# Optimization experiments

Hardware: AMD Instinct MI355X
Metric: run time of the kernel (lower is better)

## Reference

```python
import jax, jax.numpy as jnp
import numpy as np

B, S, D, H, WS = 2, 4096, 768, 12, 256
HD = D // H
NW = S // WS
EPS = 1e-5


def layernorm(x, g, b):
    mu = jnp.mean(x, axis=-1, keepdims=True)
    var = jnp.mean(jnp.square(x - mu), axis=-1, keepdims=True)
    return (x - mu) * jax.lax.rsqrt(var + EPS) * g + b


def setup_inputs() -> dict:
    key = jax.random.key(0)
    ks = jax.random.split(key, 8)
    s = 0.02
    return {
        "x": jax.random.normal(ks[0], (B, S, D), dtype=jnp.float32),
        "Wq": jax.random.normal(ks[1], (D, D), dtype=jnp.float32) * s,
        "bq": jnp.zeros((D,), jnp.float32),
        "Wk": jax.random.normal(ks[2], (D, D), dtype=jnp.float32) * s,
        "bk": jnp.zeros((D,), jnp.float32),
        "Wv": jax.random.normal(ks[3], (D, D), dtype=jnp.float32) * s,
        "bv": jnp.zeros((D,), jnp.float32),
        "Wo": jax.random.normal(ks[4], (D, D), dtype=jnp.float32) * s,
        "bo": jnp.zeros((D,), jnp.float32),
        "ln1_g": jnp.ones((D,), jnp.float32),
        "ln1_b": jnp.zeros((D,), jnp.float32),
        "W1": jax.random.normal(ks[5], (D, 4 * D), dtype=jnp.float32) * s,
        "b1": jnp.zeros((4 * D,), jnp.float32),
        "W2": jax.random.normal(ks[6], (4 * D, D), dtype=jnp.float32) * s,
        "b2": jnp.zeros((D,), jnp.float32),
        "ln2_g": jnp.ones((D,), jnp.float32),
        "ln2_b": jnp.zeros((D,), jnp.float32),
    }


def _attn(h, Wq, bq, Wk, bk, Wv, bv, Wo, bo):
    q = (h @ Wq + bq).reshape(B, S, H, HD)
    k = (h @ Wk + bk).reshape(B, S, H, HD)
    v = (h @ Wv + bv).reshape(B, S, H, HD)
    # split into windows: [B, NW, WS, H, HD]
    kb = k.reshape(B, NW, WS, H, HD)
    vb = v.reshape(B, NW, WS, H, HD)
    qw = jnp.moveaxis(q.reshape(B, NW, WS, H, HD), 1, 0)  # [NW, B, WS, H, HD]
    inv = 1.0 / np.sqrt(HD).astype(np.float32)

    def step(carry, qi_i):
        qi, i = qi_i  # qi: [B, WS, H, HD]
        # per key-window scores: [B, H, NW, WSq, WSk]
        scores = jnp.einsum('bqhd,bjkhd->bhjqk', qi, kb) * inv
        attn = jax.nn.softmax(scores, axis=-1)  # per-block softmax (as in source)
        mask = (jnp.arange(NW) <= i).astype(attn.dtype)  # block-causal, include own window
        attn = attn * mask[None, None, :, None, None]
        ctx = jnp.einsum('bhjqk,bjkhd->bqhd', attn, vb)  # sum over key windows
        return carry, ctx

    _, ctxs = jax.lax.scan(step, None, (qw, jnp.arange(NW)))
    ctx = jnp.moveaxis(ctxs, 0, 1).reshape(B, S, D)
    return ctx @ Wo + bo


def reference(x, Wq, bq, Wk, bk, Wv, bv, Wo, bo, ln1_g, ln1_b, W1, b1, W2, b2, ln2_g, ln2_b):
    attn_out = _attn(layernorm(x, ln1_g, ln1_b), Wq, bq, Wk, bk, Wv, bv, Wo, bo)
    x = x + attn_out
    h2 = layernorm(x, ln2_g, ln2_b)
    ff = jax.nn.gelu(h2 @ W1 + b1, approximate=False) @ W2 + b2
    return x + ff
```

## Files before the change

### kernel.cpp

```cpp
#include <hip/hip_runtime.h>
#include <cstdint>
#include <cstddef>

#define DEV __device__ __forceinline__

typedef unsigned short u16;
typedef unsigned int u32;
typedef __attribute__((ext_vector_type(8))) short s16x8;
typedef __attribute__((ext_vector_type(4))) float f32x4;
typedef __attribute__((ext_vector_type(4))) unsigned int u32x4;

typedef unsigned int u32_as1 __attribute__((address_space(1)));
typedef unsigned int u32_as3 __attribute__((address_space(3)));

DEV u16 f2bf(float f){
  unsigned u = __float_as_uint(f);
  u += 0x7fffu + ((u >> 16) & 1u);
  return (u16)(u >> 16);
}

DEV u32 cvtpk_bf16(float lo, float hi){
  u32 r;
  asm("v_cvt_pk_bf16_f32 %0, %1, %2" : "=v"(r) : "v"(lo), "v"(hi));
  return r;
}

DEV float fexp2(float x){
  float r;
  asm("v_exp_f32 %0, %1" : "=v"(r) : "v"(x));
  return r;
}

DEV float frcp(float x){
  float r;
  asm("v_rcp_f32 %0, %1" : "=v"(r) : "v"(x));
  return r;
}

DEV void gload16(const void* g, void* l){
  __builtin_amdgcn_global_load_lds((const u32_as1*)g, (u32_as3*)l, 16, 0, 0);
}

DEV float gelu_tanh(float x){
  float x2 = x*x;
  float z = 2.3022083f * x * fmaf(x2, 0.044715f, 1.0f);
  z = fminf(z, 100.0f);
  float t = fexp2(z);
  return x * t * frcp(t + 1.0f);
}

template<int NZ>
__global__ __launch_bounds__(256) void wconv_kernel(
    const float* __restrict__ Wa, const float* __restrict__ Wb,
    const float* __restrict__ Wc, const float* __restrict__ Wd,
    u16* __restrict__ Da, u16* __restrict__ Db, u16* __restrict__ Dc, u16* __restrict__ Dd,
    int K, int N){
  __shared__ float tl[32][33];
  int z = (NZ>1) ? blockIdx.z : 0;
  const float* W = (z==0)?Wa:(z==1)?Wb:(z==2)?Wc:Wd;
  u16* Wt = (z==0)?Da:(z==1)?Db:(z==2)?Dc:Dd;
  int tx = threadIdx.x & 31, ty = threadIdx.x >> 5;
  int k0 = blockIdx.x * 32, n0 = blockIdx.y * 32;
  #pragma unroll
  for (int p=0;p<4;p++)
    tl[ty+8*p][tx] = W[(size_t)(k0+ty+8*p)*N + (n0+tx)];
  __syncthreads();
  #pragma unroll
  for (int p=0;p<4;p++){
    int n = ty+8*p;
    Wt[(size_t)(n0+n)*K + (k0+tx)] = f2bf(tl[tx][n]);
  }
}

__global__ __launch_bounds__(256) void vconv_kernel(const u16* __restrict__ vbuf,
                                                    u16* __restrict__ vtb){
  __shared__ u16 TL[64][65];
  int t = threadIdx.x;
  int kt = blockIdx.x, bh = blockIdx.y;
  int b = bh / 12, h = bh - b*12;
  const u16* src = vbuf + ((size_t)(b*4096 + kt*64) * 768) + h*64;
  int d = t & 63, kg = t >> 6;
  #pragma unroll
  for (int j=0;j<16;j++){
    int k = kg*16 + j;
    TL[k][d] = src[(size_t)k*768 + d];
  }
  __syncthreads();
  u16* dst = vtb + ((size_t)bh*64)*4096 + (size_t)kt*64;
  #pragma unroll
  for (int it=0; it<2; it++){
    int idx = it*256 + t;
    int dd = idx >> 3, gn = idx & 7;
    s16x8 o;
    #pragma unroll
    for (int e=0;e<8;e++){
      int klocal = (gn>>2)*32 + 4*(gn&3) + (e>>1) + 16*(e&1);
      ((u16*)&o)[e] = TL[klocal][dd];
    }
    *(s16x8*)(dst + (size_t)dd*4096 + gn*8) = o;
  }
}

__global__ __launch_bounds__(256) void ln_kernel(const float* __restrict__ x,
                                                 const float* __restrict__ g,
                                                 const float* __restrict__ bta,
                                                 u16* __restrict__ out){
  int row = blockIdx.x, t = threadIdx.x;
  const float* xr = x + (size_t)row*768;
  float v0 = xr[t], v1 = xr[t+256], v2 = xr[t+512];
  float s = v0+v1+v2, s2 = v0*v0+v1*v1+v2*v2;
  #pragma unroll
  for (int m=1;m<64;m<<=1){ s += __shfl_xor(s,m); s2 += __shfl_xor(s2,m); }
  __shared__ float ls[4], ls2[4];
  int w = t>>6;
  if ((t&63)==0){ ls[w]=s; ls2[w]=s2; }
  __syncthreads();
  s = ls[0]+ls[1]+ls[2]+ls[3]; s2 = ls2[0]+ls2[1]+ls2[2]+ls2[3];
  float mu = s*(1.0f/768.0f);
  float rstd = rsqrtf(s2*(1.0f/768.0f) - mu*mu + 1e-5f);
  u16* orow = out + (size_t)row*768;
  orow[t]     = f2bf((v0-mu)*rstd*g[t]     + bta[t]);
  orow[t+256] = f2bf((v1-mu)*rstd*g[t+256] + bta[t+256]);
  orow[t+512] = f2bf((v2-mu)*rstd*g[t+512] + bta[t+512]);
}

template<bool GELU, bool RES, bool OUTBF16, int BM>
__global__ __launch_bounds__(256) void gemm_kernel(
    const u16* __restrict__ A, const u16* __restrict__ Bt0, size_t btStride,
    const float* __restrict__ bias0, const float* __restrict__ bias1, const float* __restrict__ bias2,
    const float* __restrict__ res, void* __restrict__ out0, size_t outStride,
    int M, int N, int K, float qscale)
{
  constexpr int AM = BM/32;
  __shared__ u16 As[BM*64];
  __shared__ u16 Bs[128*64];
  const int t = threadIdx.x, lane = t & 63, w = t >> 6;
  const int lj = lane & 15, g = lane >> 4;
  const int wm = w >> 1, wn = w & 1;
  const int z = blockIdx.z;
  const u16* Bt = Bt0 + (size_t)z * btStride;
  const float* bias = (z==0) ? bias0 : (z==1 ? bias1 : bias2);
  const u16* Arow = A  + (size_t)blockIdx.x * BM * K;
  const u16* Brow = Bt + (size_t)blockIdx.y * 128 * K;

  f32x4 acc[AM][4];
  #pragma unroll
  for (int a=0;a<AM;a++)
    #pragma unroll
    for (int b=0;b<4;b++){ f32x4 zz = {0.f,0.f,0.f,0.f}; acc[a][b] = zz; }

  for (int kk=0; kk<K; kk+=64){
    #pragma unroll
    for (int cc=0;cc<BM/32;cc++){
      int c = cc*256 + t;
      int row = c>>3, gp = c&7;
      gload16(Arow + (size_t)row*K + kk + ((gp ^ (row&7))<<3),
              (void*)(As + (size_t)(cc*256 + w*64)*8));
    }
    #pragma unroll
    for (int cc=0;cc<4;cc++){
      int c = cc*256 + t;
      int row = c>>3, gp = c&7;
      gload16(Brow + (size_t)row*K + kk + ((gp ^ (row&7))<<3),
              (void*)(Bs + (size_t)(cc*256 + w*64)*8));
    }
    __syncthreads();
    #pragma unroll
    for (int ks=0;ks<2;ks++){
      s16x8 af[AM], bfr[4];
      #pragma unroll
      for (int mt=0;mt<AM;mt++){
        int row = wm*(BM/2)+mt*16+lj;
        af[mt]  = *(const s16x8*)&As[(size_t)row*64 + (((ks*4+g) ^ (lj&7))<<3)];
      }
      #pragma unroll
      for (int nt=0;nt<4;nt++){
        int row = wn*64+nt*16+lj;
        bfr[nt] = *(const s16x8*)&Bs[(size_t)row*64 + (((ks*4+g) ^ (lj&7))<<3)];
      }
      #pragma unroll
      for (int mt=0;mt<AM;mt++)
        #pragma unroll
        for (int nt=0;nt<4;nt++)
          acc[mt][nt] = __builtin_amdgcn_mfma_f32_16x16x32_bf16(af[mt], bfr[nt], acc[mt][nt], 0,0,0);
    }
    __syncthreads();
  }

  const size_t gr0 = (size_t)blockIdx.x*BM + wm*(BM/2);
  const int gc0 = blockIdx.y*128 + wn*64;
  float* outF = (float*)out0; u16* outB = (u16*)out0;
  if (OUTBF16) outB += (size_t)z*outStride; else outF += (size_t)z*outStride;
  #pragma unroll
  for (int mt=0;mt<AM;mt++)
    #pragma unroll
    for (int nt=0;nt<4;nt++){
      int gc = gc0 + nt*16 + lj;
      float bv = bias[gc];
      #pragma unroll
      for (int r=0;r<4;r++){
        size_t gr = gr0 + mt*16 + g*4 + r;
        float val = acc[mt][nt][r] + bv;
        if (z==0) val *= qscale;
        if (RES)  val += res[gr*(size_t)N + gc];
        if (GELU) val = gelu_tanh(val);
        if (OUTBF16) outB[gr*(size_t)N + gc] = f2bf(val);
        else         outF[gr*(size_t)N + gc] = val;
      }
    }
}

__global__ __launch_bounds__(256,3) void attn_kernel(
    const u16* __restrict__ qb, const u16* __restrict__ kb,
    const u16* __restrict__ vtb, u16* __restrict__ ctx)
{
  __shared__ u16 KV[256*64];
  const int t = threadIdx.x, lane = t & 63, w = t >> 6;
  const int lj = lane & 15, g = lane >> 4;
  const int bx = blockIdx.x;
  const int pp = bx & 7, qq = (bx >> 3) & 3, bh = bx >> 5;
  const int h = bh % 12, b = bh / 12;
  const size_t seqbase = (size_t)b * 4096;
  const int hoff = h * 64;

  #pragma unroll
  for (int f=0; f<2; f++){
    const int iw = f ? (15 - pp) : pp;
    const int qrow0 = iw*256 + qq*64 + w*16;

    s16x8 qa[2];
    #pragma unroll
    for (int ks=0;ks<2;ks++)
      qa[ks] = *(const s16x8*)(qb + (seqbase + qrow0 + lj)*768 + hoff + ks*32 + g*8);

    f32x4 cacc[4];
    #pragma unroll
    for (int dt=0;dt<4;dt++){ f32x4 zz = {0.f,0.f,0.f,0.f}; cacc[dt] = zz; }

    for (int jw=0; jw<=iw; jw++){
      const u16* kwin = kb + (seqbase + jw*256)*768 + hoff;
      const u16* vtwin = vtb + (size_t)bh*64*4096 + jw*256;

      __syncthreads();
      #pragma unroll
      for (int cc=0;cc<8;cc++){
        int c = cc*256 + t;
        int krow = c>>3, vp = c&7;
        gload16(kwin + (size_t)krow*768 + ((vp ^ (krow&7))<<3),
                (void*)(KV + (size_t)(cc*256 + w*64)*8));
      }
      __syncthreads();

      f32x4 sacc[16];
      #pragma unroll
      for (int kt=0;kt<16;kt++){ f32x4 zz = {0.f,0.f,0.f,0.f}; sacc[kt] = zz; }
      __builtin_amdgcn_s_setprio(1);
      #pragma unroll
      for (int kt=0;kt<16;kt++){
        int kl = kt*16 + lj;
        #pragma unroll
        for (int ks=0;ks<2;ks++){
          s16x8 kf = *(const s16x8*)&KV[ (size_t)kl*64 + (((4*ks+g) ^ (kl&7))<<3) ];
          sacc[kt] = __builtin_amdgcn_mfma_f32_16x16x32_bf16(kf, qa[ks], sacc[kt], 0,0,0);
        }
      }
      __builtin_amdgcn_s_setprio(0);
      __syncthreads();

      #pragma unroll
      for (int cc=0;cc<8;cc++){
        int c = cc*256 + t;
        int d = c>>5, cp = c&31;
        gload16(vtwin + (size_t)d*4096 + ((cp ^ (d&15))<<3),
                (void*)(KV + (size_t)(cc*256 + w*64)*8));
      }

      float sm = 0.f;
      #pragma unroll
      for (int kt=0;kt<16;kt++)
        #pragma unroll
        for (int r=0;r<4;r++){
          float pv = fexp2(sacc[kt][r]);
          sacc[kt][r] = pv; sm += pv;
        }
      sm += __shfl_xor(sm, 16);
      sm += __shfl_xor(sm, 32);
      float rs = frcp(sm);

      __syncthreads();

      f32x4 pacc[4];
      #pragma unroll
      for (int dt=0;dt<4;dt++){ f32x4 zz = {0.f,0.f,0.f,0.f}; pacc[dt] = zz; }
      #pragma unroll
      for (int ks=0;ks<8;ks++){
        u32x4 pw;
        #pragma unroll
        for (int r=0;r<4;r++)
          pw[r] = cvtpk_bf16(sacc[2*ks][r], sacc[2*ks+1][r]);
        s16x8 pa = __builtin_bit_cast(s16x8, pw);
        __builtin_amdgcn_s_setprio(1);
        #pragma unroll
        for (int dt=0;dt<4;dt++){
          int d = dt*16 + lj;
          s16x8 vf = *(const s16x8*)&KV[ (size_t)d*256 + (((4*ks+g) ^ (d&15))<<3) ];
          pacc[dt] = __builtin_amdgcn_mfma_f32_16x16x32_bf16(pa, vf, pacc[dt], 0,0,0);
        }
        __builtin_amdgcn_s_setprio(0);
      }
      #pragma unroll
      for (int dt=0;dt<4;dt++)
        #pragma unroll
        for (int r=0;r<4;r++)
          cacc[dt][r] += rs * pacc[dt][r];
    }

    #pragma unroll
    for (int dt=0;dt<4;dt++)
      #pragma unroll
      for (int r=0;r<4;r++){
        int qrow = qrow0 + g*4 + r;
        ctx[ (seqbase + qrow)*768 + hoff + dt*16 + lj ] = f2bf(cacc[dt][r]);
      }
  }
}

extern "C" void kernel_launch(void* const* d_in, const int* in_sizes, int n_in,
                              void* d_out, int out_size, void* d_ws, size_t ws_size,
                              hipStream_t stream)
{
  const float* x    = (const float*)d_in[0];
  const float* Wq   = (const float*)d_in[1];
  const float* bq   = (const float*)d_in[2];
  const float* Wk   = (const float*)d_in[3];
  const float* bk   = (const float*)d_in[4];
  const float* Wv   = (const float*)d_in[5];
  const float* bv   = (const float*)d_in[6];
  const float* Wo   = (const float*)d_in[7];
  const float* bo   = (const float*)d_in[8];
  const float* ln1g = (const float*)d_in[9];
  const float* ln1b = (const float*)d_in[10];
  const float* W1   = (const float*)d_in[11];
  const float* b1   = (const float*)d_in[12];
  const float* W2   = (const float*)d_in[13];
  const float* b2   = (const float*)d_in[14];
  const float* ln2g = (const float*)d_in[15];
  const float* ln2b = (const float*)d_in[16];

  char* ws = (char*)d_ws;
  constexpr size_t SZ_W768  = (size_t)768*768*2;
  constexpr size_t SZ_W3072 = (size_t)768*3072*2;
  constexpr size_t SZ_HB    = (size_t)8192*768*2;
  u16* wtq = (u16*)(ws);
  u16* wtk = (u16*)(ws + SZ_W768);
  u16* wtv = (u16*)(ws + 2*SZ_W768);
  u16* wto = (u16*)(ws + 3*SZ_W768);
  u16* wt1 = (u16*)(ws + 4*SZ_W768);
  u16* wt2 = (u16*)(ws + 4*SZ_W768 + SZ_W3072);
  char* p0 = ws + 4*SZ_W768 + 2*SZ_W3072;
  u16*   hbuf = (u16*)p0;
  u16*   qbuf = (u16*)(p0 + SZ_HB);
  u16*   kbuf = (u16*)(p0 + 2*SZ_HB);
  u16*   vbuf = (u16*)(p0 + 3*SZ_HB);
  u16*   cbuf = (u16*)(p0 + 4*SZ_HB);
  float* x1   = (float*)(p0 + 5*SZ_HB);
  u16*   vtbuf = hbuf;
  u16*   ffa  = qbuf;
  float* outp = (float*)d_out;

  wconv_kernel<4><<<dim3(24,24,4), 256, 0, stream>>>(
      Wq, Wk, Wv, Wo, wtq, wtk, wtv, wto, 768, 768);
  wconv_kernel<1><<<dim3(24,96), 256, 0, stream>>>(
      W1, W1, W1, W1, wt1, wt1, wt1, wt1, 768, 3072);
  wconv_kernel<1><<<dim3(96,24), 256, 0, stream>>>(
      W2, W2, W2, W2, wt2, wt2, wt2, wt2, 3072, 768);

  ln_kernel<<<8192, 256, 0, stream>>>(x, ln1g, ln1b, hbuf);
  gemm_kernel<false,false,true,128><<<dim3(64,6,3), 256, 0, stream>>>(
      hbuf, wtq, (size_t)768*768, bq, bk, bv, nullptr, qbuf, (size_t)8192*768,
      8192, 768, 768, 0.180336880111f);
  vconv_kernel<<<dim3(64,24), 256, 0, stream>>>(vbuf, vtbuf);
  attn_kernel<<<768, 256, 0, stream>>>(qbuf, kbuf, vtbuf, cbuf);
  gemm_kernel<false,true,false,64><<<dim3(128,6,1), 256, 0, stream>>>(
      cbuf, wto, 0, bo, bo, bo, x, x1, 0, 8192, 768, 768, 1.0f);
  ln_kernel<<<8192, 256, 0, stream>>>(x1, ln2g, ln2b, hbuf);
  gemm_kernel<true,false,true,128><<<dim3(64,24,1), 256, 0, stream>>>(
      hbuf, wt1, 0, b1, b1, b1, nullptr, ffa, 0, 8192, 3072, 768, 1.0f);
  gemm_kernel<false,true,false,64><<<dim3(128,6,1), 256, 0, stream>>>(
      ffa, wt2, 0, b2, b2, b2, x1, outp, 0, 8192, 768, 3072, 1.0f);
}
```

Before: 275.4 us.

## Fuse V transpose into QKV GEMM epilogue and split K/V shared buffers

The QKV GEMM epilogue for the V slice now writes V directly in the transposed, permuted bf16 layout the attention kernel expects, so the separate vconv transpose kernel and its extra pass over V are removed. The attention kernel gets separate shared-memory tiles for K and V, loading both before one barrier instead of reusing one buffer with two extra syncs. This doubles LDS per block, so the occupancy hint drops from 3 to 2 blocks per CU, and the epilogue's strided 4-byte stores may coalesce less well.

```diff
diff --git a/kernel.cpp b/kernel.cpp
--- a/kernel.cpp
+++ b/kernel.cpp
@@ -72,35 +72,6 @@
   }
 }
 
-__global__ __launch_bounds__(256) void vconv_kernel(const u16* __restrict__ vbuf,
-                                                    u16* __restrict__ vtb){
-  __shared__ u16 TL[64][65];
-  int t = threadIdx.x;
-  int kt = blockIdx.x, bh = blockIdx.y;
-  int b = bh / 12, h = bh - b*12;
-  const u16* src = vbuf + ((size_t)(b*4096 + kt*64) * 768) + h*64;
-  int d = t & 63, kg = t >> 6;
-  #pragma unroll
-  for (int j=0;j<16;j++){
-    int k = kg*16 + j;
-    TL[k][d] = src[(size_t)k*768 + d];
-  }
-  __syncthreads();
-  u16* dst = vtb + ((size_t)bh*64)*4096 + (size_t)kt*64;
-  #pragma unroll
-  for (int it=0; it<2; it++){
-    int idx = it*256 + t;
-    int dd = idx >> 3, gn = idx & 7;
-    s16x8 o;
-    #pragma unroll
-    for (int e=0;e<8;e++){
-      int klocal = (gn>>2)*32 + 4*(gn&3) + (e>>1) + 16*(e&1);
-      ((u16*)&o)[e] = TL[klocal][dd];
-    }
-    *(s16x8*)(dst + (size_t)dd*4096 + gn*8) = o;
-  }
-}
-
 __global__ __launch_bounds__(256) void ln_kernel(const float* __restrict__ x,
                                                  const float* __restrict__ g,
                                                  const float* __restrict__ bta,
@@ -124,12 +95,12 @@
   orow[t+512] = f2bf((v2-mu)*rstd*g[t+512] + bta[t+512]);
 }
 
-template<bool GELU, bool RES, bool OUTBF16, int BM>
+template<bool GELU, bool RES, bool OUTBF16, int BM, bool VPERM=false>
 __global__ __launch_bounds__(256) void gemm_kernel(
     const u16* __restrict__ A, const u16* __restrict__ Bt0, size_t btStride,
     const float* __restrict__ bias0, const float* __restrict__ bias1, const float* __restrict__ bias2,
     const float* __restrict__ res, void* __restrict__ out0, size_t outStride,
-    int M, int N, int K, float qscale)
+    int M, int N, int K, float qscale, u32* __restrict__ vtb = nullptr)
 {
   constexpr int AM = BM/32;
   __shared__ u16 As[BM*64];
@@ -189,6 +160,30 @@
 
   const size_t gr0 = (size_t)blockIdx.x*BM + wm*(BM/2);
   const int gc0 = blockIdx.y*128 + wn*64;
+
+  if (VPERM && z == 2){
+    const int b_ = (int)(gr0 >> 12);
+    const int kt = (int)((gr0 & 4095) >> 6);
+    #pragma unroll
+    for (int mt2=0; mt2<AM; mt2+=2){
+      const u32 gnq = 4*(mt2>>1) + g;
+      #pragma unroll
+      for (int nt=0;nt<4;nt++){
+        int gc = gc0 + nt*16 + lj;
+        int hh = gc>>6, dd = gc&63;
+        float bv = bias[gc];
+        size_t base = ((size_t)(b_*12+hh)*64 + dd)*2048 + (size_t)kt*32 + gnq*4;
+        #pragma unroll
+        for (int r=0;r<4;r++){
+          float ve = acc[mt2][nt][r]   + bv;
+          float vo = acc[mt2+1][nt][r] + bv;
+          vtb[base + r] = cvtpk_bf16(ve, vo);
+        }
+      }
+    }
+    return;
+  }
+
   float* outF = (float*)out0; u16* outB = (u16*)out0;
   if (OUTBF16) outB += (size_t)z*outStride; else outF += (size_t)z*outStride;
   #pragma unroll
@@ -210,11 +205,12 @@
     }
 }
 
-__global__ __launch_bounds__(256,3) void attn_kernel(
+__global__ __launch_bounds__(256,2) void attn_kernel(
     const u16* __restrict__ qb, const u16* __restrict__ kb,
     const u16* __restrict__ vtb, u16* __restrict__ ctx)
 {
-  __shared__ u16 KV[256*64];
+  __shared__ u16 Ks[256*64];
+  __shared__ u16 Vs[64*256];
   const int t = threadIdx.x, lane = t & 63, w = t >> 6;
   const int lj = lane & 15, g = lane >> 4;
   const int bx = blockIdx.x;
@@ -247,33 +243,31 @@
         int c = cc*256 + t;
         int krow = c>>3, vp = c&7;
         gload16(kwin + (size_t)krow*768 + ((vp ^ (krow&7))<<3),
-                (void*)(KV + (size_t)(cc*256 + w*64)*8));
-      }
-      __syncthreads();
-
-      f32x4 sacc[16];
-      #pragma unroll
-      for (int kt=0;kt<16;kt++){ f32x4 zz = {0.f,0.f,0.f,0.f}; sacc[kt] = zz; }
-      __builtin_amdgcn_s_setprio(1);
-      #pragma unroll
-      for (int kt=0;kt<16;kt++){
-        int kl = kt*16 + lj;
-        #pragma unroll
-        for (int ks=0;ks<2;ks++){
-          s16x8 kf = *(const s16x8*)&KV[ (size_t)kl*64 + (((4*ks+g) ^ (kl&7))<<3) ];
-          sacc[kt] = __builtin_amdgcn_mfma_f32_16x16x32_bf16(kf, qa[ks], sacc[kt], 0,0,0);
-        }
-      }
-      __builtin_amdgcn_s_setprio(0);
-      __syncthreads();
-
+                (void*)(Ks + (size_t)(cc*256 + w*64)*8));
+      }
       #pragma unroll
       for (int cc=0;cc<8;cc++){
         int c = cc*256 + t;
         int d = c>>5, cp = c&31;
         gload16(vtwin + (size_t)d*4096 + ((cp ^ (d&15))<<3),
-                (void*)(KV + (size_t)(cc*256 + w*64)*8));
-      }
+                (void*)(Vs + (size_t)(cc*256 + w*64)*8));
+      }
+      __syncthreads();
+
+      f32x4 sacc[16];
+      #pragma unroll
+      for (int kt=0;kt<16;kt++){ f32x4 zz = {0.f,0.f,0.f,0.f}; sacc[kt] = zz; }
+      __builtin_amdgcn_s_setprio(1);
+      #pragma unroll
+      for (int kt=0;kt<16;kt++){
+        int kl = kt*16 + lj;
+        #pragma unroll
+        for (int ks=0;ks<2;ks++){
+          s16x8 kf = *(const s16x8*)&Ks[ (size_t)kl*64 + (((4*ks+g) ^ (kl&7))<<3) ];
+          sacc[kt] = __builtin_amdgcn_mfma_f32_16x16x32_bf16(kf, qa[ks], sacc[kt], 0,0,0);
+        }
+      }
+      __builtin_amdgcn_s_setprio(0);
 
       float sm = 0.f;
       #pragma unroll
@@ -287,8 +281,6 @@
       sm += __shfl_xor(sm, 32);
       float rs = frcp(sm);
 
-      __syncthreads();
-
       f32x4 pacc[4];
       #pragma unroll
       for (int dt=0;dt<4;dt++){ f32x4 zz = {0.f,0.f,0.f,0.f}; pacc[dt] = zz; }
@@ -303,7 +295,7 @@
         #pragma unroll
         for (int dt=0;dt<4;dt++){
           int d = dt*16 + lj;
-          s16x8 vf = *(const s16x8*)&KV[ (size_t)d*256 + (((4*ks+g) ^ (d&15))<<3) ];
+          s16x8 vf = *(const s16x8*)&Vs[ (size_t)d*256 + (((4*ks+g) ^ (d&15))<<3) ];
           pacc[dt] = __builtin_amdgcn_mfma_f32_16x16x32_bf16(pa, vf, pacc[dt], 0,0,0);
         }
         __builtin_amdgcn_s_setprio(0);
@@ -358,15 +350,14 @@
   u16* wt1 = (u16*)(ws + 4*SZ_W768);
   u16* wt2 = (u16*)(ws + 4*SZ_W768 + SZ_W3072);
   char* p0 = ws + 4*SZ_W768 + 2*SZ_W3072;
-  u16*   hbuf = (u16*)p0;
-  u16*   qbuf = (u16*)(p0 + SZ_HB);
-  u16*   kbuf = (u16*)(p0 + 2*SZ_HB);
-  u16*   vbuf = (u16*)(p0 + 3*SZ_HB);
-  u16*   cbuf = (u16*)(p0 + 4*SZ_HB);
-  float* x1   = (float*)(p0 + 5*SZ_HB);
-  u16*   vtbuf = hbuf;
-  u16*   ffa  = qbuf;
-  float* outp = (float*)d_out;
+  u16*   hbuf  = (u16*)p0;
+  u16*   qbuf  = (u16*)(p0 + SZ_HB);
+  u16*   kbuf  = (u16*)(p0 + 2*SZ_HB);
+  u16*   vtbuf = (u16*)(p0 + 3*SZ_HB);
+  u16*   cbuf  = (u16*)(p0 + 4*SZ_HB);
+  float* x1    = (float*)(p0 + 5*SZ_HB);
+  u16*   ffa   = qbuf;
+  float* outp  = (float*)d_out;
 
   wconv_kernel<4><<<dim3(24,24,4), 256, 0, stream>>>(
       Wq, Wk, Wv, Wo, wtq, wtk, wtv, wto, 768, 768);
@@ -376,10 +367,9 @@
       W2, W2, W2, W2, wt2, wt2, wt2, wt2, 3072, 768);
 
   ln_kernel<<<8192, 256, 0, stream>>>(x, ln1g, ln1b, hbuf);
-  gemm_kernel<false,false,true,128><<<dim3(64,6,3), 256, 0, stream>>>(
+  gemm_kernel<false,false,true,128,true><<<dim3(64,6,3), 256, 0, stream>>>(
       hbuf, wtq, (size_t)768*768, bq, bk, bv, nullptr, qbuf, (size_t)8192*768,
-      8192, 768, 768, 0.180336880111f);
-  vconv_kernel<<<dim3(64,24), 256, 0, stream>>>(vbuf, vtbuf);
+      8192, 768, 768, 0.180336880111f, (u32*)vtbuf);
   attn_kernel<<<768, 256, 0, stream>>>(qbuf, kbuf, vtbuf, cbuf);
   gemm_kernel<false,true,false,64><<<dim3(128,6,1), 256, 0, stream>>>(
       cbuf, wto, 0, bo, bo, bo, x, x1, 0, 8192, 768, 768, 1.0f);
```

Result: slower. 296.4 us (+7.6%).
